# Performance work log

Hardware: AMD Instinct MI355X
Metric: run time of the kernel (lower is better)

Reference implementation:

```python
import jax, jax.numpy as jnp
import numpy as np

N_CELLS = 2048
D_IN = 512
D_HID = 1024
D_OUT = 512
SYNC = 0.15
DEBATE = 0.15
N_FACTIONS = 8


def setup_inputs() -> dict:
    key = jax.random.key(0)
    ks = jax.random.split(key, 24)
    def w(k, shape, s=0.02):
        return jax.random.normal(k, shape, dtype=jnp.float32) * s
    ein = D_IN + D_HID          # complex-engine input dim (1536)
    gin = D_OUT + 1 + D_HID     # GRU gate input dim (1537)
    return {
        "x": jax.random.normal(ks[0], (1, D_IN), dtype=jnp.float32),
        "h_re": w(ks[1], (N_CELLS, D_HID), 0.1),
        "h_im": w(ks[2], (N_CELLS, D_HID), 0.1),
        "ea_wr": w(ks[3], (ein, D_OUT)), "ea_br": w(ks[4], (D_OUT,)),
        "ea_wi": w(ks[5], (ein, D_OUT)), "ea_bi": w(ks[6], (D_OUT,)),
        "eg_wr": w(ks[7], (ein, D_OUT)), "eg_br": w(ks[8], (D_OUT,)),
        "eg_wi": w(ks[9], (ein, D_OUT)), "eg_bi": w(ks[10], (D_OUT,)),
        "gz_w": w(ks[11], (gin, D_HID)), "gz_b": w(ks[12], (D_HID,)),
        "gr_w": w(ks[13], (gin, D_HID)), "gr_b": w(ks[14], (D_HID,)),
        "ghr_w": w(ks[15], (gin, D_HID)), "ghr_b": w(ks[16], (D_HID,)),
        "ghi_w": w(ks[17], (gin, D_HID)), "ghi_b": w(ks[18], (D_HID,)),
        "oh_w": w(ks[19], (2 * D_OUT, D_IN)), "oh_b": w(ks[20], (D_IN,)),
        "step": 7,
    }


def _clin(a, b, Wr, br, Wi, bi):
    # complex linear: (Wr + iWi)(a + ib) with torch's bias semantics
    return (a @ Wr + br) - (b @ Wi + bi), (b @ Wr + br) + (a @ Wi + bi)


def reference(x, h_re, h_im, ea_wr, ea_br, ea_wi, ea_bi, eg_wr, eg_br, eg_wi, eg_bi,
              gz_w, gz_b, gr_w, gr_b, ghr_w, ghr_b, ghi_w, ghi_b, oh_w, oh_b, step):
    # batch the 256-cell Python loop into single GEMMs over the cell axis
    xb = jnp.broadcast_to(x, (N_CELLS, D_IN))
    c_re = jnp.concatenate([xb, h_re], -1)                       # [N, D_IN+D_HID]
    c_im = jnp.concatenate([jnp.zeros_like(xb), h_im], -1)
    a_re, a_im = _clin(c_re, c_im, ea_wr, ea_br, ea_wi, ea_bi)
    g_re, g_im = _clin(c_re, c_im, eg_wr, eg_br, eg_wi, eg_bi)
    o_re, o_im = a_re - g_re, a_im - g_im                        # [N, D_OUT]
    tension = jnp.mean(o_re**2 + o_im**2, -1)                    # [N]

    # GRU memory update (detached input, matching output.detach())
    so_re = jax.lax.stop_gradient(o_re)
    so_im = jax.lax.stop_gradient(o_im)
    t_sg = jax.lax.stop_gradient(tension)
    mem_re = jnp.concatenate([so_re, t_sg[:, None]], -1)         # [N, D_OUT+1]
    mem_im = jnp.concatenate([so_im, jnp.zeros((N_CELLS, 1), o_im.dtype)], -1)
    x_mag = jnp.sqrt(mem_re**2 + mem_im**2)
    h_mag = jnp.sqrt(h_re**2 + h_im**2)
    cm = jnp.concatenate([x_mag, h_mag], -1)                     # [N, D_OUT+1+D_HID]
    z = jax.nn.sigmoid(cm @ gz_w + gz_b)
    r = jax.nn.sigmoid(cm @ gr_w + gr_b)
    comb_r = jnp.concatenate([mem_re, r * h_re], -1)
    comb_i = jnp.concatenate([mem_im, r * h_im], -1)
    cand_re = jnp.tanh(comb_r @ ghr_w + ghr_b)
    cand_im = jnp.tanh(comb_i @ ghi_w + ghi_b)
    nh_re = jax.lax.stop_gradient((1 - z) * h_re + z * cand_re)
    nh_im = jax.lax.stop_gradient((1 - z) * h_im + z * cand_im)

    # faction sync + debate (linear op, applied per component)
    fs = N_CELLS // N_FACTIONS
    def sync(h):
        hf = h.reshape(N_FACTIONS, fs, D_HID)
        hf = (1 - SYNC) * hf + SYNC * jnp.mean(hf, 1, keepdims=True)
        if step > 5:
            glob = jnp.mean(jnp.mean(hf, 1), 0)                  # [D_HID]
            dc = max(1, fs // 4)
            hf = hf.at[:, :dc].set((1 - DEBATE) * hf[:, :dc] + DEBATE * glob)
        return hf.reshape(N_CELLS, D_HID)
    nh_re, nh_im = sync(nh_re), sync(nh_im)

    # tension-softmax-weighted combination (weights are non-differentiable, .item() in torch)
    w_soft = jax.nn.softmax(t_sg)                                # [N]
    comb_re = (w_soft[:, None] * o_re).sum(0, keepdims=True)     # [1, D_OUT]
    comb_im = (w_soft[:, None] * o_im).sum(0, keepdims=True)
    out_real = jnp.concatenate([comb_re, comb_im], -1)           # [1, 2*D_OUT]
    pred = out_real @ oh_w + oh_b                                # [1, D_IN]
    return pred, jnp.mean(tension), nh_re, nh_im
```

## Files before the change

### kernel.cpp

```cpp
#include <hip/hip_runtime.h>
#include <math.h>

#define N_CELLS 2048
#define D_IN 512
#define D_HID 1024
#define D_OUT 512

typedef __attribute__((ext_vector_type(8))) short bf16x8;
typedef __attribute__((ext_vector_type(4))) float f32x4;
typedef __attribute__((ext_vector_type(4))) short short4v;

#define MFMA16(a, b, c) __builtin_amdgcn_mfma_f32_16x16x32_bf16(a, b, c, 0, 0, 0)

__device__ __forceinline__ short f2bf(float f) {
  union { float f; unsigned u; } v; v.f = f;
  unsigned r = (v.u + 0x7FFFu + ((v.u >> 16) & 1u)) >> 16;
  return (short)r;
}

__device__ __forceinline__ void gl_lds16(const void* g, void* l) {
  __builtin_amdgcn_global_load_lds(
      (const __attribute__((address_space(1))) void*)g,
      (__attribute__((address_space(3))) void*)l, 16, 0, 0);
}


__global__ __launch_bounds__(256) void k_transpose_wd(
    const float* __restrict__ ea_wr, const float* __restrict__ eg_wr,
    const float* __restrict__ ea_wi, const float* __restrict__ eg_wi,
    short* __restrict__ wdrT, short* __restrict__ wdiT, short* __restrict__ wdnT) {
  __shared__ float tr[32][33], ti[32][33];
  const int k0 = blockIdx.x * 32, n0 = blockIdx.y * 32;
  const int c = threadIdx.x & 31, r4 = threadIdx.x >> 5;
#pragma unroll
  for (int i = 0; i < 4; ++i) {
    int kl = r4 * 4 + i;
    int src = (512 + k0 + kl) * D_OUT + n0 + c;
    tr[kl][c] = ea_wr[src] - eg_wr[src];
    ti[kl][c] = ea_wi[src] - eg_wi[src];
  }
  __syncthreads();
#pragma unroll
  for (int i = 0; i < 4; ++i) {
    int nl = r4 * 4 + i;
    int dst = (n0 + nl) * D_HID + k0 + c;
    float dr = tr[c][nl], di = ti[c][nl];
    wdrT[dst] = f2bf(dr);
    wdiT[dst] = f2bf(di);
    wdnT[dst] = f2bf(-di);
  }
}

__global__ __launch_bounds__(256) void k_transpose_gate4(
    const float* __restrict__ w0, const float* __restrict__ w1,
    const float* __restrict__ w2, const float* __restrict__ w3,
    short* __restrict__ t0, short* __restrict__ t1,
    short* __restrict__ t2, short* __restrict__ t3) {
  const float* w = (blockIdx.z == 0) ? w0 : (blockIdx.z == 1) ? w1
                 : (blockIdx.z == 2) ? w2 : w3;
  short* wT = (blockIdx.z == 0) ? t0 : (blockIdx.z == 1) ? t1
            : (blockIdx.z == 2) ? t2 : t3;
  __shared__ float t[32][33];
  const int k0 = blockIdx.x * 32, n0 = blockIdx.y * 32;
  const int c = threadIdx.x & 31, r4 = threadIdx.x >> 5;
#pragma unroll
  for (int i = 0; i < 4; ++i) {
    int kl = r4 * 4 + i;
    int k = k0 + kl;
    int srcrow = (k < 512) ? k : k + 1;
    t[kl][c] = w[(size_t)srcrow * D_HID + n0 + c];
  }
  __syncthreads();
#pragma unroll
  for (int i = 0; i < 4; ++i) {
    int nl = r4 * 4 + i;
    wT[(size_t)(n0 + nl) * 1536 + k0 + c] = f2bf(t[c][nl]);
  }
}

__global__ __launch_bounds__(256) void k_prep_h(
    const float* __restrict__ h_re, const float* __restrict__ h_im,
    short* __restrict__ hbre, short* __restrict__ hbim, short* __restrict__ gatesA) {
  int idx4 = (blockIdx.x * 256 + threadIdx.x) * 4;
  int m = idx4 >> 10, n = idx4 & 1023;
  float4 hr = *(const float4*)&h_re[idx4];
  float4 hi = *(const float4*)&h_im[idx4];
  short4v br, bi, bm;
  br.x = f2bf(hr.x); br.y = f2bf(hr.y); br.z = f2bf(hr.z); br.w = f2bf(hr.w);
  bi.x = f2bf(hi.x); bi.y = f2bf(hi.y); bi.z = f2bf(hi.z); bi.w = f2bf(hi.w);
  bm.x = f2bf(sqrtf(hr.x * hr.x + hi.x * hi.x));
  bm.y = f2bf(sqrtf(hr.y * hr.y + hi.y * hi.y));
  bm.z = f2bf(sqrtf(hr.z * hr.z + hi.z * hi.z));
  bm.w = f2bf(sqrtf(hr.w * hr.w + hi.w * hi.w));
  *(short4v*)&hbre[idx4] = br;
  *(short4v*)&hbim[idx4] = bi;
  *(short4v*)&gatesA[(size_t)m * 1536 + 512 + n] = bm;
}

__global__ __launch_bounds__(256) void k_bias_part(
    const float* __restrict__ x,
    const float* __restrict__ ea_wr, const float* __restrict__ ea_wi,
    const float* __restrict__ eg_wr, const float* __restrict__ eg_wi,
    float* __restrict__ bpartr, float* __restrict__ bparti) {
  int n = blockIdx.x * 256 + threadIdx.x;
  int kc = blockIdx.y;
  float sr = 0.f, si = 0.f;
  for (int i = 0; i < 64; ++i) {
    int k = kc * 64 + i;
    float xv = x[k];
    int idx = k * D_OUT + n;
    sr += xv * (ea_wr[idx] - eg_wr[idx]);
    si += xv * (ea_wi[idx] - eg_wi[idx]);
  }
  bpartr[kc * D_OUT + n] = sr;
  bparti[kc * D_OUT + n] = si;
}

__global__ __launch_bounds__(256) void k_bias_red(
    const float* __restrict__ bpartr, const float* __restrict__ bparti,
    const float* __restrict__ ea_br, const float* __restrict__ ea_bi,
    const float* __restrict__ eg_br, const float* __restrict__ eg_bi,
    float* __restrict__ bias_re, float* __restrict__ bias_im) {
  int n = blockIdx.x * 256 + threadIdx.x;
  float sr = 0.f, si = 0.f;
#pragma unroll
  for (int kc = 0; kc < 8; ++kc) { sr += bpartr[kc * D_OUT + n]; si += bparti[kc * D_OUT + n]; }
  float brd = ea_br[n] - eg_br[n];
  float bid = ea_bi[n] - eg_bi[n];
  bias_re[n] = sr + brd - bid;
  bias_im[n] = si + brd + bid;
}

__global__ __launch_bounds__(256) void k_engine(
    const short* __restrict__ hbre, const short* __restrict__ hbim,
    const short* __restrict__ wdrT, const short* __restrict__ wdiT,
    const short* __restrict__ wdnT,
    const float* __restrict__ bias_re, const float* __restrict__ bias_im,
    float* __restrict__ ore, float* __restrict__ oim,
    short* __restrict__ gatesA, short* __restrict__ candAre, short* __restrict__ candAim) {
  __shared__ short Ar[128 * 32], Ai[128 * 32];
  __shared__ short Brs[64 * 32], Bis[64 * 32], Bns[64 * 32];
  const int m0 = blockIdx.x * 128, n0 = blockIdx.y * 64;
  const int tid = threadIdx.x;
  const int wid = tid >> 6, lane = tid & 63;
  const int quad = lane >> 4, lcol = lane & 15;
  const int wm = (wid >> 1) * 64, wn = (wid & 1) * 32;
  f32x4 accre[4][2], accim[4][2];
#pragma unroll
  for (int mt = 0; mt < 4; ++mt)
#pragma unroll
    for (int nt = 0; nt < 2; ++nt) {
      accre[mt][nt] = (f32x4){0.f, 0.f, 0.f, 0.f};
      accim[mt][nt] = (f32x4){0.f, 0.f, 0.f, 0.f};
    }
  for (int k0 = 0; k0 < D_HID; k0 += 32) {
    if (k0) __syncthreads();
#pragma unroll
    for (int i = 0; i < 2; ++i) {
      int c = i * 256 + tid;
      int row = c >> 2, kq = (c & 3) << 3;
      size_t goff = (size_t)(m0 + row) * D_HID + k0 + kq;
      gl_lds16(hbre + goff, &Ar[c * 8]);
      gl_lds16(hbim + goff, &Ai[c * 8]);
    }
    {
      int row = tid >> 2, kq = (tid & 3) << 3;
      size_t goff = (size_t)(n0 + row) * D_HID + k0 + kq;
      gl_lds16(wdrT + goff, &Brs[tid * 8]);
      gl_lds16(wdiT + goff, &Bis[tid * 8]);
      gl_lds16(wdnT + goff, &Bns[tid * 8]);
    }
    __syncthreads();
    bf16x8 ar[4], ai[4], br[2], bi[2], bn[2];
#pragma unroll
    for (int mt = 0; mt < 4; ++mt) {
      int off = (wm + mt * 16 + lcol) * 32 + quad * 8;
      ar[mt] = *(const bf16x8*)&Ar[off];
      ai[mt] = *(const bf16x8*)&Ai[off];
    }
#pragma unroll
    for (int nt = 0; nt < 2; ++nt) {
      int off = (wn + nt * 16 + lcol) * 32 + quad * 8;
      br[nt] = *(const bf16x8*)&Brs[off];
      bi[nt] = *(const bf16x8*)&Bis[off];
      bn[nt] = *(const bf16x8*)&Bns[off];
    }
#pragma unroll
    for (int mt = 0; mt < 4; ++mt)
#pragma unroll
      for (int nt = 0; nt < 2; ++nt) {
        accre[mt][nt] = MFMA16(ar[mt], br[nt], accre[mt][nt]);
        accre[mt][nt] = MFMA16(ai[mt], bn[nt], accre[mt][nt]);
        accim[mt][nt] = MFMA16(ar[mt], bi[nt], accim[mt][nt]);
        accim[mt][nt] = MFMA16(ai[mt], br[nt], accim[mt][nt]);
      }
  }
#pragma unroll
  for (int mt = 0; mt < 4; ++mt)
#pragma unroll
    for (int nt = 0; nt < 2; ++nt)
#pragma unroll
      for (int r = 0; r < 4; ++r) {
        int m = m0 + wm + mt * 16 + quad * 4 + r;
        int n = n0 + wn + nt * 16 + lcol;
        float cre = accre[mt][nt][r] + bias_re[n];
        float cim = accim[mt][nt][r] + bias_im[n];
        ore[(size_t)m * D_OUT + n] = cre;
        oim[(size_t)m * D_OUT + n] = cim;
        gatesA[(size_t)m * 1536 + n] = f2bf(sqrtf(cre * cre + cim * cim));
        candAre[(size_t)m * 1536 + n] = f2bf(cre);
        candAim[(size_t)m * 1536 + n] = f2bf(cim);
      }
}

__global__ __launch_bounds__(256) void k_tension(
    const float* __restrict__ ore, const float* __restrict__ oim,
    float* __restrict__ tens) {
  int m = blockIdx.x, tid = threadIdx.x;
  float s = 0.f;
  for (int k = tid; k < D_OUT; k += 256) {
    float a = ore[(size_t)m * D_OUT + k], b = oim[(size_t)m * D_OUT + k];
    s += a * a + b * b;
  }
  for (int off = 32; off; off >>= 1) s += __shfl_down(s, off);
  __shared__ float red[4];
  if ((tid & 63) == 0) red[tid >> 6] = s;
  __syncthreads();
  if (tid == 0) tens[m] = (red[0] + red[1] + red[2] + red[3]) * (1.f / D_OUT);
}

__global__ __launch_bounds__(256) void k_gates(
    const short* __restrict__ gatesA,
    const short* __restrict__ gzwT, const short* __restrict__ grwT,
    const float* __restrict__ gz_w, const float* __restrict__ gz_b,
    const float* __restrict__ gr_w, const float* __restrict__ gr_b,
    const float* __restrict__ tens,
    const float* __restrict__ h_re, const float* __restrict__ h_im,
    float* __restrict__ zbuf,
    short* __restrict__ candAre, short* __restrict__ candAim) {
  __shared__ short As[128 * 32];
  __shared__ short Bzs[64 * 32], Brs[64 * 32];
  const int m0 = blockIdx.x * 128, n0 = blockIdx.y * 64;
  const int tid = threadIdx.x;
  const int wid = tid >> 6, lane = tid & 63;
  const int quad = lane >> 4, lcol = lane & 15;
  const int wm = (wid >> 1) * 64, wn = (wid & 1) * 32;
  f32x4 az[4][2], aq[4][2];
#pragma unroll
  for (int mt = 0; mt < 4; ++mt)
#pragma unroll
    for (int nt = 0; nt < 2; ++nt) {
      az[mt][nt] = (f32x4){0.f, 0.f, 0.f, 0.f};
      aq[mt][nt] = (f32x4){0.f, 0.f, 0.f, 0.f};
    }
  for (int k0 = 0; k0 < 1536; k0 += 32) {
    if (k0) __syncthreads();
#pragma unroll
    for (int i = 0; i < 2; ++i) {
      int c = i * 256 + tid;
      int row = c >> 2, kq = (c & 3) << 3;
      gl_lds16(gatesA + (size_t)(m0 + row) * 1536 + k0 + kq, &As[c * 8]);
    }
    {
      int row = tid >> 2, kq = (tid & 3) << 3;
      size_t goff = (size_t)(n0 + row) * 1536 + k0 + kq;
      gl_lds16(gzwT + goff, &Bzs[tid * 8]);
      gl_lds16(grwT + goff, &Brs[tid * 8]);
    }
    __syncthreads();
    bf16x8 a[4], bz[2], bq[2];
#pragma unroll
    for (int mt = 0; mt < 4; ++mt)
      a[mt] = *(const bf16x8*)&As[(wm + mt * 16 + lcol) * 32 + quad * 8];
#pragma unroll
    for (int nt = 0; nt < 2; ++nt) {
      int off = (wn + nt * 16 + lcol) * 32 + quad * 8;
      bz[nt] = *(const bf16x8*)&Bzs[off];
      bq[nt] = *(const bf16x8*)&Brs[off];
    }
#pragma unroll
    for (int mt = 0; mt < 4; ++mt)
#pragma unroll
      for (int nt = 0; nt < 2; ++nt) {
        az[mt][nt] = MFMA16(a[mt], bz[nt], az[mt][nt]);
        aq[mt][nt] = MFMA16(a[mt], bq[nt], aq[mt][nt]);
      }
  }
#pragma unroll
  for (int mt = 0; mt < 4; ++mt)
#pragma unroll
    for (int nt = 0; nt < 2; ++nt)
#pragma unroll
      for (int r = 0; r < 4; ++r) {
        int m = m0 + wm + mt * 16 + quad * 4 + r;
        int n = n0 + wn + nt * 16 + lcol;
        float tv = tens[m];
        float zp = az[mt][nt][r] + gz_b[n] + tv * gz_w[(size_t)512 * D_HID + n];
        float rp = aq[mt][nt][r] + gr_b[n] + tv * gr_w[(size_t)512 * D_HID + n];
        float z = 1.f / (1.f + expf(-zp));
        float rr = 1.f / (1.f + expf(-rp));
        zbuf[(size_t)m * D_HID + n] = z;
        candAre[(size_t)m * 1536 + 512 + n] = f2bf(rr * h_re[(size_t)m * D_HID + n]);
        candAim[(size_t)m * 1536 + 512 + n] = f2bf(rr * h_im[(size_t)m * D_HID + n]);
      }
}

__global__ __launch_bounds__(256) void k_cand(
    const short* __restrict__ candAre, const short* __restrict__ candAim,
    const short* __restrict__ ghrwT, const short* __restrict__ ghiwT,
    const float* __restrict__ ghr_b, const float* __restrict__ ghi_b,
    const float* __restrict__ ghr_w,
    const float* __restrict__ tens, const float* __restrict__ zbuf,
    const float* __restrict__ h_re, const float* __restrict__ h_im,
    float* __restrict__ nhre, float* __restrict__ nhim) {
  __shared__ short As[128 * 32];
  __shared__ short Bs[64 * 32];
  const int is_re = (blockIdx.z == 0);
  const short* A = is_re ? candAre : candAim;
  const short* Bt = is_re ? ghrwT : ghiwT;
  const float* bias = is_re ? ghr_b : ghi_b;
  const float* h = is_re ? h_re : h_im;
  float* outp = is_re ? nhre : nhim;
  const int m0 = blockIdx.x * 128, n0 = blockIdx.y * 64;
  const int tid = threadIdx.x;
  const int wid = tid >> 6, lane = tid & 63;
  const int quad = lane >> 4, lcol = lane & 15;
  const int wm = (wid >> 1) * 64, wn = (wid & 1) * 32;
  f32x4 acc[4][2];
#pragma unroll
  for (int mt = 0; mt < 4; ++mt)
#pragma unroll
    for (int nt = 0; nt < 2; ++nt) acc[mt][nt] = (f32x4){0.f, 0.f, 0.f, 0.f};
  for (int k0 = 0; k0 < 1536; k0 += 32) {
    if (k0) __syncthreads();
#pragma unroll
    for (int i = 0; i < 2; ++i) {
      int c = i * 256 + tid;
      int row = c >> 2, kq = (c & 3) << 3;
      gl_lds16(A + (size_t)(m0 + row) * 1536 + k0 + kq, &As[c * 8]);
    }
    {
      int row = tid >> 2, kq = (tid & 3) << 3;
      gl_lds16(Bt + (size_t)(n0 + row) * 1536 + k0 + kq, &Bs[tid * 8]);
    }
    __syncthreads();
    bf16x8 a[4], b[2];
#pragma unroll
    for (int mt = 0; mt < 4; ++mt)
      a[mt] = *(const bf16x8*)&As[(wm + mt * 16 + lcol) * 32 + quad * 8];
#pragma unroll
    for (int nt = 0; nt < 2; ++nt)
      b[nt] = *(const bf16x8*)&Bs[(wn + nt * 16 + lcol) * 32 + quad * 8];
#pragma unroll
    for (int mt = 0; mt < 4; ++mt)
#pragma unroll
      for (int nt = 0; nt < 2; ++nt)
        acc[mt][nt] = MFMA16(a[mt], b[nt], acc[mt][nt]);
  }
#pragma unroll
  for (int mt = 0; mt < 4; ++mt)
#pragma unroll
    for (int nt = 0; nt < 2; ++nt)
#pragma unroll
      for (int r = 0; r < 4; ++r) {
        int m = m0 + wm + mt * 16 + quad * 4 + r;
        int n = n0 + wn + nt * 16 + lcol;
        float pre = acc[mt][nt][r] + bias[n];
        if (is_re) pre += tens[m] * ghr_w[(size_t)512 * D_HID + n];
        float cand = tanhf(pre);
        float z = zbuf[(size_t)m * D_HID + n];
        float hv = h[(size_t)m * D_HID + n];
        outp[(size_t)m * D_HID + n] = (1.f - z) * hv + z * cand;
      }
}

__global__ __launch_bounds__(256) void k_fsum_part(
    const float* __restrict__ nhre, const float* __restrict__ nhim,
    float* __restrict__ fpart) {
  int f = blockIdx.x >> 3, rc = blockIdx.x & 7, comp = blockIdx.y;
  const float* src = comp ? nhim : nhre;
  int row0 = f * 256 + rc * 32;
#pragma unroll
  for (int nc = 0; nc < 4; ++nc) {
    int n = nc * 256 + threadIdx.x;
    float s = 0.f;
    const float* base = src + (size_t)row0 * D_HID + n;
    for (int j = 0; j < 32; ++j) s += base[(size_t)j * D_HID];
    fpart[((size_t)comp * 64 + blockIdx.x) * D_HID + n] = s;
  }
}

__global__ __launch_bounds__(256) void k_fsum_red(
    const float* __restrict__ fpart,
    float* __restrict__ fsre, float* __restrict__ fsim,
    float* __restrict__ gre, float* __restrict__ gim) {
  int n = blockIdx.x * 256 + threadIdx.x;
  int comp = blockIdx.y;
  float* fs = comp ? fsim : fsre;
  float* g = comp ? gim : gre;
  float gsum = 0.f;
#pragma unroll
  for (int f = 0; f < 8; ++f) {
    float sf = 0.f;
#pragma unroll
    for (int rc = 0; rc < 8; ++rc)
      sf += fpart[((size_t)comp * 64 + f * 8 + rc) * D_HID + n];
    fs[f * D_HID + n] = sf;
    gsum += sf;
  }
  g[n] = gsum * (1.f / 2048.f);
}

__global__ __launch_bounds__(256) void k_sync(
    float* __restrict__ nhre, float* __restrict__ nhim,
    const float* __restrict__ fsre, const float* __restrict__ fsim,
    const float* __restrict__ gre, const float* __restrict__ gim,
    const int* __restrict__ step) {
  int idx = blockIdx.x * 256 + threadIdx.x;
  int m = idx >> 10, n = idx & 1023;
  int f = m >> 8;
  float vr = nhre[idx], vi = nhim[idx];
  vr = 0.85f * vr + 0.15f * (fsre[f * D_HID + n] * (1.f / 256.f));
  vi = 0.85f * vi + 0.15f * (fsim[f * D_HID + n] * (1.f / 256.f));
  if (step[0] > 5 && (m & 255) < 64) {
    vr = 0.85f * vr + 0.15f * gre[n];
    vi = 0.85f * vi + 0.15f * gim[n];
  }
  nhre[idx] = vr;
  nhim[idx] = vi;
}

__global__ __launch_bounds__(1024) void k_stats(
    const float* __restrict__ tens, float* __restrict__ wsoft,
    float* __restrict__ meanT_out) {
  __shared__ float red[16];
  __shared__ float s_max, s_sum;
  int tid = threadIdx.x;
  int wid = tid >> 6, lane = tid & 63;
  float a = tens[tid], b = tens[tid + 1024];
  float mx = fmaxf(a, b);
  for (int off = 32; off; off >>= 1) mx = fmaxf(mx, __shfl_down(mx, off));
  if (lane == 0) red[wid] = mx;
  __syncthreads();
  if (tid == 0) {
    float m2 = red[0];
    for (int i = 1; i < 16; ++i) m2 = fmaxf(m2, red[i]);
    s_max = m2;
  }
  __syncthreads();
  float mxv = s_max;
  float ea = expf(a - mxv), eb = expf(b - mxv);
  float se = ea + eb;
  for (int off = 32; off; off >>= 1) se += __shfl_down(se, off);
  __syncthreads();
  if (lane == 0) red[wid] = se;
  __syncthreads();
  if (tid == 0) {
    float s2 = 0.f;
    for (int i = 0; i < 16; ++i) s2 += red[i];
    s_sum = s2;
  }
  __syncthreads();
  float inv = 1.f / s_sum;
  wsoft[tid] = ea * inv;
  wsoft[tid + 1024] = eb * inv;
  float st = a + b;
  for (int off = 32; off; off >>= 1) st += __shfl_down(st, off);
  __syncthreads();
  if (lane == 0) red[wid] = st;
  __syncthreads();
  if (tid == 0) {
    float s2 = 0.f;
    for (int i = 0; i < 16; ++i) s2 += red[i];
    meanT_out[0] = s2 * (1.f / 2048.f);
  }
}

__global__ __launch_bounds__(256) void k_comb_part(
    const float* __restrict__ ore, const float* __restrict__ oim,
    const float* __restrict__ wsoft, float* __restrict__ cpart) {
  int j = blockIdx.x * 256 + threadIdx.x;
  int mc = blockIdx.y;
  const float* src = (j < 512) ? ore : oim;
  int col = j & 511;
  float s = 0.f;
  for (int i = 0; i < 128; ++i) {
    int m = mc * 128 + i;
    s += wsoft[m] * src[(size_t)m * D_OUT + col];
  }
  cpart[(size_t)mc * 1024 + j] = s;
}

__global__ __launch_bounds__(256) void k_comb_red(
    const float* __restrict__ cpart, float* __restrict__ comb) {
  int j = blockIdx.x * 256 + threadIdx.x;
  float s = 0.f;
#pragma unroll
  for (int mc = 0; mc < 16; ++mc) s += cpart[(size_t)mc * 1024 + j];
  comb[j] = s;
}

__global__ __launch_bounds__(256) void k_pred_part(
    const float* __restrict__ comb, const float* __restrict__ oh_w,
    float* __restrict__ ppart) {
  int n = blockIdx.x * 256 + threadIdx.x;
  int jc = blockIdx.y;
  float s = 0.f;
  for (int i = 0; i < 128; ++i) {
    int j = jc * 128 + i;
    s += comb[j] * oh_w[(size_t)j * D_IN + n];
  }
  ppart[(size_t)jc * D_IN + n] = s;
}

__global__ __launch_bounds__(256) void k_pred_red(
    const float* __restrict__ ppart, const float* __restrict__ oh_b,
    float* __restrict__ pred) {
  int n = blockIdx.x * 256 + threadIdx.x;
  float s = oh_b[n];
#pragma unroll
  for (int jc = 0; jc < 8; ++jc) s += ppart[(size_t)jc * D_IN + n];
  pred[n] = s;
}

extern "C" void kernel_launch(void* const* d_in, const int* in_sizes, int n_in,
                              void* d_out, int out_size, void* d_ws, size_t ws_size,
                              hipStream_t stream) {
  const float* x     = (const float*)d_in[0];
  const float* h_re  = (const float*)d_in[1];
  const float* h_im  = (const float*)d_in[2];
  const float* ea_wr = (const float*)d_in[3];
  const float* ea_br = (const float*)d_in[4];
  const float* ea_wi = (const float*)d_in[5];
  const float* ea_bi = (const float*)d_in[6];
  const float* eg_wr = (const float*)d_in[7];
  const float* eg_br = (const float*)d_in[8];
  const float* eg_wi = (const float*)d_in[9];
  const float* eg_bi = (const float*)d_in[10];
  const float* gz_w  = (const float*)d_in[11];
  const float* gz_b  = (const float*)d_in[12];
  const float* gr_w  = (const float*)d_in[13];
  const float* gr_b  = (const float*)d_in[14];
  const float* ghr_w = (const float*)d_in[15];
  const float* ghr_b = (const float*)d_in[16];
  const float* ghi_w = (const float*)d_in[17];
  const float* ghi_b = (const float*)d_in[18];
  const float* oh_w  = (const float*)d_in[19];
  const float* oh_b  = (const float*)d_in[20];
  const int*   step  = (const int*)d_in[21];

  float* out = (float*)d_out;
  float* pred_out  = out;
  float* meanT_out = out + 512;
  float* nhre_out  = out + 513;
  float* nhim_out  = out + 513 + N_CELLS * D_HID;

  char* p = (char*)d_ws;
  auto carve = [&](size_t bytes) { char* r = p; p += (bytes + 255) & ~(size_t)255; return r; };
  short* wdrT   = (short*)carve(512 * 1024 * 2);
  short* wdiT   = (short*)carve(512 * 1024 * 2);
  short* wdnT   = (short*)carve(512 * 1024 * 2);
  short* gzwT   = (short*)carve(1024 * 1536 * 2);
  short* grwT   = (short*)carve(1024 * 1536 * 2);
  short* ghrwT  = (short*)carve(1024 * 1536 * 2);
  short* ghiwT  = (short*)carve(1024 * 1536 * 2);
  short* hbre   = (short*)carve(2048 * 1024 * 2);
  short* hbim   = (short*)carve(2048 * 1024 * 2);
  short* gatesA = (short*)carve((size_t)2048 * 1536 * 2);
  short* candAre= (short*)carve((size_t)2048 * 1536 * 2);
  short* candAim= (short*)carve((size_t)2048 * 1536 * 2);
  float* ore    = (float*)carve(2048 * 512 * 4);
  float* oim    = (float*)carve(2048 * 512 * 4);
  float* zbuf   = (float*)carve((size_t)2048 * 1024 * 4);
  float* bias_re= (float*)carve(512 * 4);
  float* bias_im= (float*)carve(512 * 4);
  float* bpartr = (float*)carve(8 * 512 * 4);
  float* bparti = (float*)carve(8 * 512 * 4);
  float* tens   = (float*)carve(2048 * 4);
  float* fpart  = (float*)carve(2 * 64 * 1024 * 4);
  float* fsre   = (float*)carve(8 * 1024 * 4);
  float* fsim   = (float*)carve(8 * 1024 * 4);
  float* gre    = (float*)carve(1024 * 4);
  float* gim    = (float*)carve(1024 * 4);
  float* wsoft  = (float*)carve(2048 * 4);
  float* cpart  = (float*)carve(16 * 1024 * 4);
  float* comb   = (float*)carve(1024 * 4);
  float* ppart  = (float*)carve(8 * 512 * 4);

  hipLaunchKernelGGL(k_transpose_wd, dim3(32, 16), dim3(256), 0, stream,
                     ea_wr, eg_wr, ea_wi, eg_wi, wdrT, wdiT, wdnT);
  hipLaunchKernelGGL(k_transpose_gate4, dim3(48, 32, 4), dim3(256), 0, stream,
                     gz_w, gr_w, ghr_w, ghi_w, gzwT, grwT, ghrwT, ghiwT);
  hipLaunchKernelGGL(k_prep_h, dim3(2048), dim3(256), 0, stream,
                     h_re, h_im, hbre, hbim, gatesA);
  hipLaunchKernelGGL(k_bias_part, dim3(2, 8), dim3(256), 0, stream,
                     x, ea_wr, ea_wi, eg_wr, eg_wi, bpartr, bparti);
  hipLaunchKernelGGL(k_bias_red, dim3(2), dim3(256), 0, stream,
                     bpartr, bparti, ea_br, ea_bi, eg_br, eg_bi, bias_re, bias_im);
  hipLaunchKernelGGL(k_engine, dim3(16, 8), dim3(256), 0, stream,
                     hbre, hbim, wdrT, wdiT, wdnT, bias_re, bias_im,
                     ore, oim, gatesA, candAre, candAim);
  hipLaunchKernelGGL(k_tension, dim3(2048), dim3(256), 0, stream, ore, oim, tens);
  hipLaunchKernelGGL(k_gates, dim3(16, 16), dim3(256), 0, stream,
                     gatesA, gzwT, grwT, gz_w, gz_b, gr_w, gr_b, tens,
                     h_re, h_im, zbuf, candAre, candAim);
  hipLaunchKernelGGL(k_cand, dim3(16, 16, 2), dim3(256), 0, stream,
                     candAre, candAim, ghrwT, ghiwT, ghr_b, ghi_b, ghr_w,
                     tens, zbuf, h_re, h_im, nhre_out, nhim_out);
  hipLaunchKernelGGL(k_fsum_part, dim3(64, 2), dim3(256), 0, stream,
                     nhre_out, nhim_out, fpart);
  hipLaunchKernelGGL(k_fsum_red, dim3(4, 2), dim3(256), 0, stream,
                     fpart, fsre, fsim, gre, gim);
  hipLaunchKernelGGL(k_sync, dim3((N_CELLS * D_HID) / 256), dim3(256), 0, stream,
                     nhre_out, nhim_out, fsre, fsim, gre, gim, step);
  hipLaunchKernelGGL(k_stats, dim3(1), dim3(1024), 0, stream, tens, wsoft, meanT_out);
  hipLaunchKernelGGL(k_comb_part, dim3(4, 16), dim3(256), 0, stream,
                     ore, oim, wsoft, cpart);
  hipLaunchKernelGGL(k_comb_red, dim3(4), dim3(256), 0, stream, cpart, comb);
  hipLaunchKernelGGL(k_pred_part, dim3(2, 8), dim3(256), 0, stream, comb, oh_w, ppart);
  hipLaunchKernelGGL(k_pred_red, dim3(2), dim3(256), 0, stream, ppart, oh_b, pred_out);
}
```

Baseline: 320.1 us.

## Fuse transposes, tension and comb reductions; retile engine and split gate GEMM

Merges the two weight-transpose kernels into one launch. Folds the tension row reduction into the engine epilogue with shuffles and atomics, zeroing the buffer in prep_h. Shrinks the engine tile to 64x32 so it runs 512 blocks, and splits the gate GEMM over blockIdx.z so z and r run as separate blocks. Doubles the K step to 64 in the engine, gate and cand GEMMs, and folds the comb reduction into pred_part. The aim is fewer launches and better CU occupancy, at the cost of float atomics, which make tension non-deterministic, and a gate A-tile that is now loaded twice.

```diff
diff --git a/kernel.cpp b/kernel.cpp
--- a/kernel.cpp
+++ b/kernel.cpp
@@ -24,63 +24,63 @@
       (__attribute__((address_space(3))) void*)l, 16, 0, 0);
 }
 
-
-__global__ __launch_bounds__(256) void k_transpose_wd(
+__global__ __launch_bounds__(256) void k_transpose_all(
+    const float* __restrict__ w0, const float* __restrict__ w1,
+    const float* __restrict__ w2, const float* __restrict__ w3,
+    short* __restrict__ t0, short* __restrict__ t1,
+    short* __restrict__ t2, short* __restrict__ t3,
     const float* __restrict__ ea_wr, const float* __restrict__ eg_wr,
     const float* __restrict__ ea_wi, const float* __restrict__ eg_wi,
     short* __restrict__ wdrT, short* __restrict__ wdiT, short* __restrict__ wdnT) {
-  __shared__ float tr[32][33], ti[32][33];
   const int k0 = blockIdx.x * 32, n0 = blockIdx.y * 32;
   const int c = threadIdx.x & 31, r4 = threadIdx.x >> 5;
-#pragma unroll
-  for (int i = 0; i < 4; ++i) {
-    int kl = r4 * 4 + i;
-    int src = (512 + k0 + kl) * D_OUT + n0 + c;
-    tr[kl][c] = ea_wr[src] - eg_wr[src];
-    ti[kl][c] = ea_wi[src] - eg_wi[src];
-  }
-  __syncthreads();
-#pragma unroll
-  for (int i = 0; i < 4; ++i) {
-    int nl = r4 * 4 + i;
-    int dst = (n0 + nl) * D_HID + k0 + c;
-    float dr = tr[c][nl], di = ti[c][nl];
-    wdrT[dst] = f2bf(dr);
-    wdiT[dst] = f2bf(di);
-    wdnT[dst] = f2bf(-di);
-  }
-}
-
-__global__ __launch_bounds__(256) void k_transpose_gate4(
-    const float* __restrict__ w0, const float* __restrict__ w1,
-    const float* __restrict__ w2, const float* __restrict__ w3,
-    short* __restrict__ t0, short* __restrict__ t1,
-    short* __restrict__ t2, short* __restrict__ t3) {
-  const float* w = (blockIdx.z == 0) ? w0 : (blockIdx.z == 1) ? w1
-                 : (blockIdx.z == 2) ? w2 : w3;
-  short* wT = (blockIdx.z == 0) ? t0 : (blockIdx.z == 1) ? t1
-            : (blockIdx.z == 2) ? t2 : t3;
-  __shared__ float t[32][33];
-  const int k0 = blockIdx.x * 32, n0 = blockIdx.y * 32;
-  const int c = threadIdx.x & 31, r4 = threadIdx.x >> 5;
-#pragma unroll
-  for (int i = 0; i < 4; ++i) {
-    int kl = r4 * 4 + i;
-    int k = k0 + kl;
-    int srcrow = (k < 512) ? k : k + 1;
-    t[kl][c] = w[(size_t)srcrow * D_HID + n0 + c];
-  }
-  __syncthreads();
-#pragma unroll
-  for (int i = 0; i < 4; ++i) {
-    int nl = r4 * 4 + i;
-    wT[(size_t)(n0 + nl) * 1536 + k0 + c] = f2bf(t[c][nl]);
+  if (blockIdx.z < 4) {
+    const float* w = (blockIdx.z == 0) ? w0 : (blockIdx.z == 1) ? w1
+                   : (blockIdx.z == 2) ? w2 : w3;
+    short* wT = (blockIdx.z == 0) ? t0 : (blockIdx.z == 1) ? t1
+              : (blockIdx.z == 2) ? t2 : t3;
+    __shared__ float t[32][33];
+#pragma unroll
+    for (int i = 0; i < 4; ++i) {
+      int kl = r4 * 4 + i;
+      int k = k0 + kl;
+      int srcrow = (k < 512) ? k : k + 1;
+      t[kl][c] = w[(size_t)srcrow * D_HID + n0 + c];
+    }
+    __syncthreads();
+#pragma unroll
+    for (int i = 0; i < 4; ++i) {
+      int nl = r4 * 4 + i;
+      wT[(size_t)(n0 + nl) * 1536 + k0 + c] = f2bf(t[c][nl]);
+    }
+  } else {
+    if (blockIdx.x >= 32 || blockIdx.y >= 16) return;
+    __shared__ float tr[32][33], ti[32][33];
+#pragma unroll
+    for (int i = 0; i < 4; ++i) {
+      int kl = r4 * 4 + i;
+      int src = (512 + k0 + kl) * D_OUT + n0 + c;
+      tr[kl][c] = ea_wr[src] - eg_wr[src];
+      ti[kl][c] = ea_wi[src] - eg_wi[src];
+    }
+    __syncthreads();
+#pragma unroll
+    for (int i = 0; i < 4; ++i) {
+      int nl = r4 * 4 + i;
+      int dst = (n0 + nl) * D_HID + k0 + c;
+      float dr = tr[c][nl], di = ti[c][nl];
+      wdrT[dst] = f2bf(dr);
+      wdiT[dst] = f2bf(di);
+      wdnT[dst] = f2bf(-di);
+    }
   }
 }
 
 __global__ __launch_bounds__(256) void k_prep_h(
     const float* __restrict__ h_re, const float* __restrict__ h_im,
-    short* __restrict__ hbre, short* __restrict__ hbim, short* __restrict__ gatesA) {
+    short* __restrict__ hbre, short* __restrict__ hbim, short* __restrict__ gatesA,
+    float* __restrict__ tens) {
+  if (threadIdx.x == 0) tens[blockIdx.x] = 0.f;
   int idx4 = (blockIdx.x * 256 + threadIdx.x) * 4;
   int m = idx4 >> 10, n = idx4 & 1023;
   float4 hr = *(const float4*)&h_re[idx4];
@@ -137,96 +137,82 @@
     const short* __restrict__ wdnT,
     const float* __restrict__ bias_re, const float* __restrict__ bias_im,
     float* __restrict__ ore, float* __restrict__ oim,
-    short* __restrict__ gatesA, short* __restrict__ candAre, short* __restrict__ candAim) {
-  __shared__ short Ar[128 * 32], Ai[128 * 32];
-  __shared__ short Brs[64 * 32], Bis[64 * 32], Bns[64 * 32];
-  const int m0 = blockIdx.x * 128, n0 = blockIdx.y * 64;
+    short* __restrict__ gatesA, short* __restrict__ candAre, short* __restrict__ candAim,
+    float* __restrict__ tens) {
+  __shared__ short Ar[2 * 64 * 32], Ai[2 * 64 * 32];
+  __shared__ short Brs[2 * 32 * 32], Bis[2 * 32 * 32], Bns[2 * 32 * 32];
+  const int m0 = blockIdx.x * 64, n0 = blockIdx.y * 32;
   const int tid = threadIdx.x;
   const int wid = tid >> 6, lane = tid & 63;
   const int quad = lane >> 4, lcol = lane & 15;
-  const int wm = (wid >> 1) * 64, wn = (wid & 1) * 32;
-  f32x4 accre[4][2], accim[4][2];
-#pragma unroll
-  for (int mt = 0; mt < 4; ++mt)
-#pragma unroll
-    for (int nt = 0; nt < 2; ++nt) {
-      accre[mt][nt] = (f32x4){0.f, 0.f, 0.f, 0.f};
-      accim[mt][nt] = (f32x4){0.f, 0.f, 0.f, 0.f};
-    }
-  for (int k0 = 0; k0 < D_HID; k0 += 32) {
+  const int wm = wid * 16;
+  f32x4 accre[2], accim[2];
+#pragma unroll
+  for (int nt = 0; nt < 2; ++nt) {
+    accre[nt] = (f32x4){0.f, 0.f, 0.f, 0.f};
+    accim[nt] = (f32x4){0.f, 0.f, 0.f, 0.f};
+  }
+  for (int k0 = 0; k0 < D_HID; k0 += 64) {
     if (k0) __syncthreads();
 #pragma unroll
     for (int i = 0; i < 2; ++i) {
       int c = i * 256 + tid;
-      int row = c >> 2, kq = (c & 3) << 3;
-      size_t goff = (size_t)(m0 + row) * D_HID + k0 + kq;
-      gl_lds16(hbre + goff, &Ar[c * 8]);
-      gl_lds16(hbim + goff, &Ai[c * 8]);
+      int kh = c >> 8, row = (c >> 2) & 63, kq = c & 3;
+      size_t g = (size_t)(m0 + row) * D_HID + k0 + kh * 32 + kq * 8;
+      gl_lds16(hbre + g, &Ar[c * 8]);
+      gl_lds16(hbim + g, &Ai[c * 8]);
     }
     {
-      int row = tid >> 2, kq = (tid & 3) << 3;
-      size_t goff = (size_t)(n0 + row) * D_HID + k0 + kq;
-      gl_lds16(wdrT + goff, &Brs[tid * 8]);
-      gl_lds16(wdiT + goff, &Bis[tid * 8]);
-      gl_lds16(wdnT + goff, &Bns[tid * 8]);
+      int c = tid;
+      int kh = c >> 7, row = (c >> 2) & 31, kq = c & 3;
+      size_t g = (size_t)(n0 + row) * D_HID + k0 + kh * 32 + kq * 8;
+      gl_lds16(wdrT + g, &Brs[c * 8]);
+      gl_lds16(wdiT + g, &Bis[c * 8]);
+      gl_lds16(wdnT + g, &Bns[c * 8]);
     }
     __syncthreads();
-    bf16x8 ar[4], ai[4], br[2], bi[2], bn[2];
-#pragma unroll
-    for (int mt = 0; mt < 4; ++mt) {
-      int off = (wm + mt * 16 + lcol) * 32 + quad * 8;
-      ar[mt] = *(const bf16x8*)&Ar[off];
-      ai[mt] = *(const bf16x8*)&Ai[off];
-    }
+#pragma unroll
+    for (int kh = 0; kh < 2; ++kh) {
+      bf16x8 ar, ai, br[2], bi[2], bn[2];
+      int aoff = kh * 2048 + (wm + lcol) * 32 + quad * 8;
+      ar = *(const bf16x8*)&Ar[aoff];
+      ai = *(const bf16x8*)&Ai[aoff];
+#pragma unroll
+      for (int nt = 0; nt < 2; ++nt) {
+        int boff = kh * 1024 + (nt * 16 + lcol) * 32 + quad * 8;
+        br[nt] = *(const bf16x8*)&Brs[boff];
+        bi[nt] = *(const bf16x8*)&Bis[boff];
+        bn[nt] = *(const bf16x8*)&Bns[boff];
+      }
+#pragma unroll
+      for (int nt = 0; nt < 2; ++nt) {
+        accre[nt] = MFMA16(ar, br[nt], accre[nt]);
+        accre[nt] = MFMA16(ai, bn[nt], accre[nt]);
+        accim[nt] = MFMA16(ar, bi[nt], accim[nt]);
+        accim[nt] = MFMA16(ai, br[nt], accim[nt]);
+      }
+    }
+  }
+#pragma unroll
+  for (int r = 0; r < 4; ++r) {
+    int m = m0 + wm + quad * 4 + r;
+    float t = 0.f;
 #pragma unroll
     for (int nt = 0; nt < 2; ++nt) {
-      int off = (wn + nt * 16 + lcol) * 32 + quad * 8;
-      br[nt] = *(const bf16x8*)&Brs[off];
-      bi[nt] = *(const bf16x8*)&Bis[off];
-      bn[nt] = *(const bf16x8*)&Bns[off];
-    }
-#pragma unroll
-    for (int mt = 0; mt < 4; ++mt)
-#pragma unroll
-      for (int nt = 0; nt < 2; ++nt) {
-        accre[mt][nt] = MFMA16(ar[mt], br[nt], accre[mt][nt]);
-        accre[mt][nt] = MFMA16(ai[mt], bn[nt], accre[mt][nt]);
-        accim[mt][nt] = MFMA16(ar[mt], bi[nt], accim[mt][nt]);
-        accim[mt][nt] = MFMA16(ai[mt], br[nt], accim[mt][nt]);
-      }
-  }
-#pragma unroll
-  for (int mt = 0; mt < 4; ++mt)
-#pragma unroll
-    for (int nt = 0; nt < 2; ++nt)
-#pragma unroll
-      for (int r = 0; r < 4; ++r) {
-        int m = m0 + wm + mt * 16 + quad * 4 + r;
-        int n = n0 + wn + nt * 16 + lcol;
-        float cre = accre[mt][nt][r] + bias_re[n];
-        float cim = accim[mt][nt][r] + bias_im[n];
-        ore[(size_t)m * D_OUT + n] = cre;
-        oim[(size_t)m * D_OUT + n] = cim;
-        gatesA[(size_t)m * 1536 + n] = f2bf(sqrtf(cre * cre + cim * cim));
-        candAre[(size_t)m * 1536 + n] = f2bf(cre);
-        candAim[(size_t)m * 1536 + n] = f2bf(cim);
-      }
-}
-
-__global__ __launch_bounds__(256) void k_tension(
-    const float* __restrict__ ore, const float* __restrict__ oim,
-    float* __restrict__ tens) {
-  int m = blockIdx.x, tid = threadIdx.x;
-  float s = 0.f;
-  for (int k = tid; k < D_OUT; k += 256) {
-    float a = ore[(size_t)m * D_OUT + k], b = oim[(size_t)m * D_OUT + k];
-    s += a * a + b * b;
-  }
-  for (int off = 32; off; off >>= 1) s += __shfl_down(s, off);
-  __shared__ float red[4];
-  if ((tid & 63) == 0) red[tid >> 6] = s;
-  __syncthreads();
-  if (tid == 0) tens[m] = (red[0] + red[1] + red[2] + red[3]) * (1.f / D_OUT);
+      int n = n0 + nt * 16 + lcol;
+      float cre = accre[nt][r] + bias_re[n];
+      float cim = accim[nt][r] + bias_im[n];
+      t += cre * cre + cim * cim;
+      ore[(size_t)m * D_OUT + n] = cre;
+      oim[(size_t)m * D_OUT + n] = cim;
+      gatesA[(size_t)m * 1536 + n] = f2bf(sqrtf(cre * cre + cim * cim));
+      candAre[(size_t)m * 1536 + n] = f2bf(cre);
+      candAim[(size_t)m * 1536 + n] = f2bf(cim);
+    }
+#pragma unroll
+    for (int off = 1; off < 16; off <<= 1) t += __shfl_xor(t, off);
+    if (lcol == 0) atomicAdd(&tens[m], t * (1.f / 512.f));
+  }
 }
 
 __global__ __launch_bounds__(256) void k_gates(
@@ -238,53 +224,50 @@
     const float* __restrict__ h_re, const float* __restrict__ h_im,
     float* __restrict__ zbuf,
     short* __restrict__ candAre, short* __restrict__ candAim) {
-  __shared__ short As[128 * 32];
-  __shared__ short Bzs[64 * 32], Brs[64 * 32];
+  __shared__ short As[2 * 128 * 32];
+  __shared__ short Bs[2 * 64 * 32];
+  const int is_z = (blockIdx.z == 0);
+  const short* Bt = is_z ? gzwT : grwT;
   const int m0 = blockIdx.x * 128, n0 = blockIdx.y * 64;
   const int tid = threadIdx.x;
   const int wid = tid >> 6, lane = tid & 63;
   const int quad = lane >> 4, lcol = lane & 15;
   const int wm = (wid >> 1) * 64, wn = (wid & 1) * 32;
-  f32x4 az[4][2], aq[4][2];
+  f32x4 acc[4][2];
 #pragma unroll
   for (int mt = 0; mt < 4; ++mt)
 #pragma unroll
-    for (int nt = 0; nt < 2; ++nt) {
-      az[mt][nt] = (f32x4){0.f, 0.f, 0.f, 0.f};
-      aq[mt][nt] = (f32x4){0.f, 0.f, 0.f, 0.f};
-    }
-  for (int k0 = 0; k0 < 1536; k0 += 32) {
+    for (int nt = 0; nt < 2; ++nt) acc[mt][nt] = (f32x4){0.f, 0.f, 0.f, 0.f};
+  for (int k0 = 0; k0 < 1536; k0 += 64) {
     if (k0) __syncthreads();
+#pragma unroll
+    for (int i = 0; i < 4; ++i) {
+      int c = i * 256 + tid;
+      int kh = c >> 9, row = (c >> 2) & 127, kq = c & 3;
+      gl_lds16(gatesA + (size_t)(m0 + row) * 1536 + k0 + kh * 32 + kq * 8, &As[c * 8]);
+    }
 #pragma unroll
     for (int i = 0; i < 2; ++i) {
       int c = i * 256 + tid;
-      int row = c >> 2, kq = (c & 3) << 3;
-      gl_lds16(gatesA + (size_t)(m0 + row) * 1536 + k0 + kq, &As[c * 8]);
-    }
-    {
-      int row = tid >> 2, kq = (tid & 3) << 3;
-      size_t goff = (size_t)(n0 + row) * 1536 + k0 + kq;
-      gl_lds16(gzwT + goff, &Bzs[tid * 8]);
-      gl_lds16(grwT + goff, &Brs[tid * 8]);
+      int kh = c >> 8, row = (c >> 2) & 63, kq = c & 3;
+      gl_lds16(Bt + (size_t)(n0 + row) * 1536 + k0 + kh * 32 + kq * 8, &Bs[c * 8]);
     }
     __syncthreads();
-    bf16x8 a[4], bz[2], bq[2];
-#pragma unroll
-    for (int mt = 0; mt < 4; ++mt)
-      a[mt] = *(const bf16x8*)&As[(wm + mt * 16 + lcol) * 32 + quad * 8];
-#pragma unroll
-    for (int nt = 0; nt < 2; ++nt) {
-      int off = (wn + nt * 16 + lcol) * 32 + quad * 8;
-      bz[nt] = *(const bf16x8*)&Bzs[off];
-      bq[nt] = *(const bf16x8*)&Brs[off];
-    }
-#pragma unroll
-    for (int mt = 0; mt < 4; ++mt)
-#pragma unroll
-      for (int nt = 0; nt < 2; ++nt) {
-        az[mt][nt] = MFMA16(a[mt], bz[nt], az[mt][nt]);
-        aq[mt][nt] = MFMA16(a[mt], bq[nt], aq[mt][nt]);
-      }
+#pragma unroll
+    for (int kh = 0; kh < 2; ++kh) {
+      bf16x8 a[4], b[2];
+#pragma unroll
+      for (int mt = 0; mt < 4; ++mt)
+        a[mt] = *(const bf16x8*)&As[kh * 4096 + (wm + mt * 16 + lcol) * 32 + quad * 8];
+#pragma unroll
+      for (int nt = 0; nt < 2; ++nt)
+        b[nt] = *(const bf16x8*)&Bs[kh * 2048 + (wn + nt * 16 + lcol) * 32 + quad * 8];
+#pragma unroll
+      for (int mt = 0; mt < 4; ++mt)
+#pragma unroll
+        for (int nt = 0; nt < 2; ++nt)
+          acc[mt][nt] = MFMA16(a[mt], b[nt], acc[mt][nt]);
+    }
   }
 #pragma unroll
   for (int mt = 0; mt < 4; ++mt)
@@ -295,13 +278,15 @@
         int m = m0 + wm + mt * 16 + quad * 4 + r;
         int n = n0 + wn + nt * 16 + lcol;
         float tv = tens[m];
-        float zp = az[mt][nt][r] + gz_b[n] + tv * gz_w[(size_t)512 * D_HID + n];
-        float rp = aq[mt][nt][r] + gr_b[n] + tv * gr_w[(size_t)512 * D_HID + n];
-        float z = 1.f / (1.f + expf(-zp));
-        float rr = 1.f / (1.f + expf(-rp));
-        zbuf[(size_t)m * D_HID + n] = z;
-        candAre[(size_t)m * 1536 + 512 + n] = f2bf(rr * h_re[(size_t)m * D_HID + n]);
-        candAim[(size_t)m * 1536 + 512 + n] = f2bf(rr * h_im[(size_t)m * D_HID + n]);
+        if (is_z) {
+          float zp = acc[mt][nt][r] + gz_b[n] + tv * gz_w[(size_t)512 * D_HID + n];
+          zbuf[(size_t)m * D_HID + n] = 1.f / (1.f + expf(-zp));
+        } else {
+          float rp = acc[mt][nt][r] + gr_b[n] + tv * gr_w[(size_t)512 * D_HID + n];
+          float rr = 1.f / (1.f + expf(-rp));
+          candAre[(size_t)m * 1536 + 512 + n] = f2bf(rr * h_re[(size_t)m * D_HID + n]);
+          candAim[(size_t)m * 1536 + 512 + n] = f2bf(rr * h_im[(size_t)m * D_HID + n]);
+        }
       }
 }
 
@@ -313,8 +298,8 @@
     const float* __restrict__ tens, const float* __restrict__ zbuf,
     const float* __restrict__ h_re, const float* __restrict__ h_im,
     float* __restrict__ nhre, float* __restrict__ nhim) {
-  __shared__ short As[128 * 32];
-  __shared__ short Bs[64 * 32];
+  __shared__ short As[2 * 128 * 32];
+  __shared__ short Bs[2 * 64 * 32];
   const int is_re = (blockIdx.z == 0);
   const short* A = is_re ? candAre : candAim;
   const short* Bt = is_re ? ghrwT : ghiwT;
@@ -331,31 +316,36 @@
   for (int mt = 0; mt < 4; ++mt)
 #pragma unroll
     for (int nt = 0; nt < 2; ++nt) acc[mt][nt] = (f32x4){0.f, 0.f, 0.f, 0.f};
-  for (int k0 = 0; k0 < 1536; k0 += 32) {
+  for (int k0 = 0; k0 < 1536; k0 += 64) {
     if (k0) __syncthreads();
+#pragma unroll
+    for (int i = 0; i < 4; ++i) {
+      int c = i * 256 + tid;
+      int kh = c >> 9, row = (c >> 2) & 127, kq = c & 3;
+      gl_lds16(A + (size_t)(m0 + row) * 1536 + k0 + kh * 32 + kq * 8, &As[c * 8]);
+    }
 #pragma unroll
     for (int i = 0; i < 2; ++i) {
       int c = i * 256 + tid;
-      int row = c >> 2, kq = (c & 3) << 3;
-      gl_lds16(A + (size_t)(m0 + row) * 1536 + k0 + kq, &As[c * 8]);
-    }
-    {
-      int row = tid >> 2, kq = (tid & 3) << 3;
-      gl_lds16(Bt + (size_t)(n0 + row) * 1536 + k0 + kq, &Bs[tid * 8]);
+      int kh = c >> 8, row = (c >> 2) & 63, kq = c & 3;
+      gl_lds16(Bt + (size_t)(n0 + row) * 1536 + k0 + kh * 32 + kq * 8, &Bs[c * 8]);
     }
     __syncthreads();
-    bf16x8 a[4], b[2];
-#pragma unroll
-    for (int mt = 0; mt < 4; ++mt)
-      a[mt] = *(const bf16x8*)&As[(wm + mt * 16 + lcol) * 32 + quad * 8];
-#pragma unroll
-    for (int nt = 0; nt < 2; ++nt)
-      b[nt] = *(const bf16x8*)&Bs[(wn + nt * 16 + lcol) * 32 + quad * 8];
-#pragma unroll
-    for (int mt = 0; mt < 4; ++mt)
+#pragma unroll
+    for (int kh = 0; kh < 2; ++kh) {
+      bf16x8 a[4], b[2];
+#pragma unroll
+      for (int mt = 0; mt < 4; ++mt)
+        a[mt] = *(const bf16x8*)&As[kh * 4096 + (wm + mt * 16 + lcol) * 32 + quad * 8];
 #pragma unroll
       for (int nt = 0; nt < 2; ++nt)
-        acc[mt][nt] = MFMA16(a[mt], b[nt], acc[mt][nt]);
+        b[nt] = *(const bf16x8*)&Bs[kh * 2048 + (wn + nt * 16 + lcol) * 32 + quad * 8];
+#pragma unroll
+      for (int mt = 0; mt < 4; ++mt)
+#pragma unroll
+        for (int nt = 0; nt < 2; ++nt)
+          acc[mt][nt] = MFMA16(a[mt], b[nt], acc[mt][nt]);
+    }
   }
 #pragma unroll
   for (int mt = 0; mt < 4; ++mt)
@@ -491,25 +481,23 @@
   cpart[(size_t)mc * 1024 + j] = s;
 }
 
-__global__ __launch_bounds__(256) void k_comb_red(
-    const float* __restrict__ cpart, float* __restrict__ comb) {
-  int j = blockIdx.x * 256 + threadIdx.x;
+__global__ __launch_bounds__(256) void k_pred_part(
+    const float* __restrict__ cpart, const float* __restrict__ oh_w,
+    float* __restrict__ ppart) {
+  __shared__ float combs[128];
+  int tid = threadIdx.x;
+  int jc = blockIdx.y;
+  if (tid < 128) {
+    float s = 0.f;
+#pragma unroll
+    for (int mc = 0; mc < 16; ++mc) s += cpart[(size_t)mc * 1024 + jc * 128 + tid];
+    combs[tid] = s;
+  }
+  __syncthreads();
+  int n = blockIdx.x * 256 + tid;
   float s = 0.f;
-#pragma unroll
-  for (int mc = 0; mc < 16; ++mc) s += cpart[(size_t)mc * 1024 + j];
-  comb[j] = s;
-}
-
-__global__ __launch_bounds__(256) void k_pred_part(
-    const float* __restrict__ comb, const float* __restrict__ oh_w,
-    float* __restrict__ ppart) {
-  int n = blockIdx.x * 256 + threadIdx.x;
-  int jc = blockIdx.y;
-  float s = 0.f;
-  for (int i = 0; i < 128; ++i) {
-    int j = jc * 128 + i;
-    s += comb[j] * oh_w[(size_t)j * D_IN + n];
-  }
+  for (int i = 0; i < 128; ++i)
+    s += combs[i] * oh_w[(size_t)(jc * 128 + i) * D_IN + n];
   ppart[(size_t)jc * D_IN + n] = s;
 }
 
@@ -584,24 +572,21 @@
   float* gim    = (float*)carve(1024 * 4);
   float* wsoft  = (float*)carve(2048 * 4);
   float* cpart  = (float*)carve(16 * 1024 * 4);
-  float* comb   = (float*)carve(1024 * 4);
   float* ppart  = (float*)carve(8 * 512 * 4);
 
-  hipLaunchKernelGGL(k_transpose_wd, dim3(32, 16), dim3(256), 0, stream,
+  hipLaunchKernelGGL(k_transpose_all, dim3(48, 32, 5), dim3(256), 0, stream,
+                     gz_w, gr_w, ghr_w, ghi_w, gzwT, grwT, ghrwT, ghiwT,
                      ea_wr, eg_wr, ea_wi, eg_wi, wdrT, wdiT, wdnT);
-  hipLaunchKernelGGL(k_transpose_gate4, dim3(48, 32, 4), dim3(256), 0, stream,
-                     gz_w, gr_w, ghr_w, ghi_w, gzwT, grwT, ghrwT, ghiwT);
   hipLaunchKernelGGL(k_prep_h, dim3(2048), dim3(256), 0, stream,
-                     h_re, h_im, hbre, hbim, gatesA);
+                     h_re, h_im, hbre, hbim, gatesA, tens);
   hipLaunchKernelGGL(k_bias_part, dim3(2, 8), dim3(256), 0, stream,
                      x, ea_wr, ea_wi, eg_wr, eg_wi, bpartr, bparti);
   hipLaunchKernelGGL(k_bias_red, dim3(2), dim3(256), 0, stream,
                      bpartr, bparti, ea_br, ea_bi, eg_br, eg_bi, bias_re, bias_im);
-  hipLaunchKernelGGL(k_engine, dim3(16, 8), dim3(256), 0, stream,
+  hipLaunchKernelGGL(k_engine, dim3(32, 16), dim3(256), 0, stream,
                      hbre, hbim, wdrT, wdiT, wdnT, bias_re, bias_im,
-                     ore, oim, gatesA, candAre, candAim);
-  hipLaunchKernelGGL(k_tension, dim3(2048), dim3(256), 0, stream, ore, oim, tens);
-  hipLaunchKernelGGL(k_gates, dim3(16, 16), dim3(256), 0, stream,
+                     ore, oim, gatesA, candAre, candAim, tens);
+  hipLaunchKernelGGL(k_gates, dim3(16, 16, 2), dim3(256), 0, stream,
                      gatesA, gzwT, grwT, gz_w, gz_b, gr_w, gr_b, tens,
                      h_re, h_im, zbuf, candAre, candAim);
   hipLaunchKernelGGL(k_cand, dim3(16, 16, 2), dim3(256), 0, stream,
@@ -616,7 +601,6 @@
   hipLaunchKernelGGL(k_stats, dim3(1), dim3(1024), 0, stream, tens, wsoft, meanT_out);
   hipLaunchKernelGGL(k_comb_part, dim3(4, 16), dim3(256), 0, stream,
                      ore, oim, wsoft, cpart);
-  hipLaunchKernelGGL(k_comb_red, dim3(4), dim3(256), 0, stream, cpart, comb);
-  hipLaunchKernelGGL(k_pred_part, dim3(2, 8), dim3(256), 0, stream, comb, oh_w, ppart);
+  hipLaunchKernelGGL(k_pred_part, dim3(2, 8), dim3(256), 0, stream, cpart, oh_w, ppart);
   hipLaunchKernelGGL(k_pred_red, dim3(2), dim3(256), 0, stream, ppart, oh_b, pred_out);
 }
```

Measured after the change: 290.9 us. 1.1x faster.
